# Performance work log

Hardware: AMD Instinct MI355X
Metric: run time of the kernel (lower is better)

## Reference

```python
import jax, jax.numpy as jnp
import numpy as np

KERNEL_SIZES = [1, 2, 3]
KERNEL_NUM = 11
SIGMA = 0.1
EXACT_SIGMA = 0.001
EMBED_DIM = 300
HIDDEN = 128
Q_VOCAB = 30000
D_VOCAB = 30000


def _mus_sigmas():
    mus, sigmas = [], []
    K = KERNEL_NUM
    for i in range(K):
        mu = 1.0 / (K - 1) + 2.0 * i / (K - 1) - 1.0
        sigma = SIGMA
        if mu > 1.0:
            sigma = EXACT_SIGMA
            mu = 1.0
        mus.append(mu)
        sigmas.append(sigma)
    return jnp.asarray(mus, jnp.float32), jnp.asarray(sigmas, jnp.float32)


def _conv_tanh(x_bcl, w, b, ks):
    # x_bcl: (B, C_in, L); ConstantPad1d((0, ks)) + Conv1d(kernel=ks+1) keeps length L
    y = jax.lax.conv_general_dilated(
        x_bcl, w, window_strides=(1,), padding=[(0, ks)],
        dimension_numbers=('NCW', 'OIW', 'NCW'))
    return jnp.tanh(y + b[None, :, None])  # (B, H, L)


def _l2norm(x):
    n = jnp.sqrt(jnp.sum(x * x, axis=-1, keepdims=True))
    return x / jnp.maximum(n, 1e-12)


def setup_inputs() -> dict:
    key = jax.random.key(0)
    ks = jax.random.split(key, 16)
    inp = {
        'query': jax.random.randint(ks[0], (128, 128), 0, Q_VOCAB),
        'doc': jax.random.randint(ks[1], (128, 512), 0, D_VOCAB),
        'q_emb': jax.random.normal(ks[2], (Q_VOCAB, EMBED_DIM), jnp.float32) * 0.1,
        'd_emb': jax.random.normal(ks[3], (D_VOCAB, EMBED_DIM), jnp.float32) * 0.1,
        'out_w': jax.random.normal(ks[4], (1, 3 * 3 * KERNEL_NUM), jnp.float32) * 0.1,
        'out_b': jnp.zeros((1,), jnp.float32),
    }
    for idx, k in enumerate(KERNEL_SIZES):
        fan_in = EMBED_DIM * (k + 1)
        inp[f'conv_w{idx}'] = jax.random.normal(ks[5 + 2 * idx], (HIDDEN, EMBED_DIM, k + 1), jnp.float32) / np.sqrt(fan_in)
        inp[f'conv_b{idx}'] = jnp.zeros((HIDDEN,), jnp.float32)
    return inp


def reference(query, doc, q_emb, d_emb, conv_w0, conv_b0, conv_w1, conv_b1,
              conv_w2, conv_b2, out_w, out_b):
    mus, sigmas = _mus_sigmas()
    inv2s2 = 1.0 / (2.0 * sigmas * sigmas)  # (K,)

    q_e = q_emb[query].transpose(0, 2, 1)  # (B, D, Lq)
    d_e = d_emb[doc].transpose(0, 2, 1)    # (B, D, Ld)

    cws = [(conv_w0, conv_b0), (conv_w1, conv_b1), (conv_w2, conv_b2)]
    # q_convs/d_convs share weights (same nn.Sequential appended to both lists)
    q_convs = [_l2norm(_conv_tanh(q_e, w, b, ks).transpose(0, 2, 1))
               for (w, b), ks in zip(cws, KERNEL_SIZES)]  # each (B, Lq, H)
    d_convs = [_l2norm(_conv_tanh(d_e, w, b, ks).transpose(0, 2, 1))
               for (w, b), ks in zip(cws, KERNEL_SIZES)]  # each (B, Ld, H)

    KM = []
    for qi in range(3):
        for di in range(3):
            mm = jnp.einsum('bld,brd->blr', q_convs[qi], d_convs[di])  # (B,Lq,Ld)
            # Gaussian kernel soft-histogram, vectorized over all kernels
            kern = jnp.exp(-(mm[..., None] - mus) ** 2 * inv2s2)  # (B,Lq,Ld,K)
            K = jnp.log1p(kern.sum(axis=2)).sum(axis=1)           # (B,K)
            KM.append(K)
    phi = jnp.concatenate(KM, axis=1)  # (B, 9*KERNEL_NUM)
    return phi @ out_w.T + out_b       # (B, 1)
```

## Files before the change

kernel.cpp:

```cpp
#include <hip/hip_runtime.h>
#include <hip/hip_bf16.h>

typedef __hip_bfloat16 bf16;
typedef __attribute__((ext_vector_type(8))) short short8;
typedef __attribute__((ext_vector_type(4))) float f32x4;
typedef __attribute__((ext_vector_type(2))) float f32x2;

#define NB 128
#define NH 128
#define NLQ 128
#define NLD 512
#define NEMB 300
#define XQROWS 132
#define XDROWS 516
#define XCOLS 320

__device__ __forceinline__ unsigned short bfbits(float x) {
    __hip_bfloat16 h = __float2bfloat16(x);
    return *reinterpret_cast<unsigned short*>(&h);
}

__device__ __forceinline__ float fast_tanh(float x) {
    x = fminf(9.f, fmaxf(-9.f, x));
    float e = __builtin_amdgcn_exp2f(x * 2.8853900817779268f);
    return (e - 1.f) * __builtin_amdgcn_rcpf(e + 1.f);
}

__global__ __launch_bounds__(256)
void pack_all(const int* __restrict__ q_tok, const int* __restrict__ d_tok,
              const float* __restrict__ q_emb, const float* __restrict__ d_emb,
              const float* __restrict__ cw0, const float* __restrict__ cw1,
              const float* __restrict__ cw2,
              bf16* __restrict__ Wp, bf16* __restrict__ Xq, bf16* __restrict__ Xd)
{
    int bx = blockIdx.x;
    if (bx < 1440) {
        int e = bx * 256 + threadIdx.x;
        int widx = (e >= 204800) ? 2 : (e >= 81920 ? 1 : 0);
        int off = (widx == 0) ? 0 : (widx == 1 ? 81920 : 204800);
        int el = e - off;
        int W = widx + 2;
        int ch = el >> 12;
        int cc = ch / W;
        int t  = ch - cc * W;
        int h  = (el >> 5) & 127;
        int cp = el & 31;
        int c  = cc * 32 + cp;
        const float* cw = (widx == 0) ? cw0 : (widx == 1 ? cw1 : cw2);
        float v = (c < NEMB) ? cw[(h * NEMB + c) * W + t] : 0.f;
        Wp[e] = __float2bfloat16(v);
        return;
    }
    int gid = (bx - 1440) * 256 + threadIdx.x;
    int row = gid / 20, g = gid - row * 20;
    const float* emb; bf16* dst; int tok;
    if (row < NB * XQROWS) {
        int b = row / XQROWS, l = row - b * XQROWS;
        tok = (l < NLQ) ? q_tok[b * NLQ + l] : -1;
        emb = q_emb;
        dst = Xq + (size_t)row * XCOLS + g * 16;
    } else {
        int rowd = row - NB * XQROWS;
        int b = rowd / XDROWS, l = rowd - b * XDROWS;
        tok = (l < NLD) ? d_tok[b * NLD + l] : -1;
        emb = d_emb;
        dst = Xd + (size_t)rowd * XCOLS + g * 16;
    }
    int c0 = g * 16;
    float4 v[4];
    #pragma unroll
    for (int q = 0; q < 4; ++q) {
        int c = c0 + q * 4;
        v[q] = make_float4(0.f, 0.f, 0.f, 0.f);
        if (tok >= 0 && c < NEMB)
            v[q] = *reinterpret_cast<const float4*>(emb + (size_t)tok * NEMB + c);
    }
    short8 o0, o1;
    o0[0] = (short)bfbits(v[0].x); o0[1] = (short)bfbits(v[0].y);
    o0[2] = (short)bfbits(v[0].z); o0[3] = (short)bfbits(v[0].w);
    o0[4] = (short)bfbits(v[1].x); o0[5] = (short)bfbits(v[1].y);
    o0[6] = (short)bfbits(v[1].z); o0[7] = (short)bfbits(v[1].w);
    o1[0] = (short)bfbits(v[2].x); o1[1] = (short)bfbits(v[2].y);
    o1[2] = (short)bfbits(v[2].z); o1[3] = (short)bfbits(v[2].w);
    o1[4] = (short)bfbits(v[3].x); o1[5] = (short)bfbits(v[3].y);
    o1[6] = (short)bfbits(v[3].z); o1[7] = (short)bfbits(v[3].w);
    *reinterpret_cast<short8*>(dst) = o0;
    *reinterpret_cast<short8*>(dst + 8) = o1;
}

__global__ __launch_bounds__(512, 4)
void conv_kernel(const bf16* __restrict__ Xq, const bf16* __restrict__ Xd,
                 const bf16* __restrict__ Wp,
                 const float* __restrict__ cb0, const float* __restrict__ cb1,
                 const float* __restrict__ cb2,
                 bf16* __restrict__ qn, bf16* __restrict__ dn)
{
    __shared__ bf16 Xs[2][2][132][40];
    __shared__ bf16 Bs[2][128][36];
    __shared__ float ssq[2][256];

    int bx = blockIdx.x;
    int widx = bx % 3;
    int inner = bx / 3;
    int W = widx + 2;
    const bf16* wp = Wp + ((widx == 0) ? 0 : (widx == 1 ? 81920 : 204800));
    const float* cb = (widx == 0) ? cb0 : (widx == 1 ? cb1 : cb2);

    int tid = threadIdx.x;
    int lane = tid & 63;
    int wv = tid >> 6;
    int wr = wv >> 1;
    int wc = wv & 1;
    int s_wave = wr >> 1;
    int lr_base = (wr & 1) * 64;

    bf16* outp; int L;
    int sb0, sb1, sl00, sl01;
    const bf16* xbase;
    size_t grow0, grow1;
    if (inner < 64) {
        outp = qn + (size_t)widx * NB * NLQ * NH;
        L = NLQ; sb0 = inner * 2; sb1 = sb0 + 1; sl00 = 0; sl01 = 0;
        xbase = Xq; grow0 = (size_t)sb0 * XQROWS; grow1 = (size_t)sb1 * XQROWS;
    } else {
        int i = inner - 64;
        outp = dn + (size_t)widx * NB * NLD * NH;
        L = NLD; sb0 = i >> 1; sb1 = sb0; sl00 = (i & 1) * 256; sl01 = sl00 + 128;
        xbase = Xd; grow0 = (size_t)sb0 * XDROWS + sl00; grow1 = grow0 + 128;
    }

    int sr = tid >> 2;
    int colg = tid & 3;
    const bf16* gsrc0 = xbase + (grow0 + sr) * XCOLS + colg * 8;
    const bf16* gsrc1 = xbase + (grow1 + sr) * XCOLS + colg * 8;
    bool has_tail = (tid >= 448 && tid < 480);
    int j = tid - 448;
    int ts = (j >> 2) >> 2, trr = 128 + ((j >> 2) & 3), tcolg = j & 3;
    const bf16* gsrcT = xbase + ((ts ? grow1 : grow0) + trr) * XCOLS + tcolg * 8;

    const short8* wp8 = reinterpret_cast<const short8*>(wp);
    int bh = tid >> 2, bcg = tid & 3;

    {
        short8 a0 = *reinterpret_cast<const short8*>(gsrc0);
        short8 a1 = *reinterpret_cast<const short8*>(gsrc1);
        short8 at;
        if (has_tail) at = *reinterpret_cast<const short8*>(gsrcT);
        short8 b0 = wp8[tid];
        *reinterpret_cast<short8*>(&Xs[0][0][sr][colg * 8]) = a0;
        *reinterpret_cast<short8*>(&Xs[0][1][sr][colg * 8]) = a1;
        if (has_tail) *reinterpret_cast<short8*>(&Xs[0][ts][trr][tcolg * 8]) = at;
        *reinterpret_cast<short8*>(&Bs[0][bh][bcg * 8]) = b0;
    }
    __syncthreads();

    f32x4 acc[4][4];
    #pragma unroll
    for (int m = 0; m < 4; ++m)
        #pragma unroll
        for (int n = 0; n < 4; ++n)
            acc[m][n] = (f32x4){0.f, 0.f, 0.f, 0.f};

    int nsteps = W * 10;
    int xcur = 0, bcur = 0, step = 0;
    short8 a0, a1, at;
    for (int cc = 0; cc < 10; ++cc) {
        if (cc < 9) {
            a0 = *reinterpret_cast<const short8*>(gsrc0 + (cc + 1) * 32);
            a1 = *reinterpret_cast<const short8*>(gsrc1 + (cc + 1) * 32);
            if (has_tail) at = *reinterpret_cast<const short8*>(gsrcT + (cc + 1) * 32);
        }
        for (int t = 0; t < W; ++t, ++step) {
            short8 nb;
            bool hn = (step + 1 < nsteps);
            if (hn) nb = wp8[(size_t)(step + 1) * 512 + tid];

            short8 bv[4], af[4];
            #pragma unroll
            for (int n = 0; n < 4; ++n)
                bv[n] = *reinterpret_cast<const short8*>(
                    &Bs[bcur][wc * 64 + n * 16 + (lane & 15)][(lane >> 4) * 8]);
            #pragma unroll
            for (int m = 0; m < 4; ++m)
                af[m] = *reinterpret_cast<const short8*>(
                    &Xs[xcur][s_wave][lr_base + m * 16 + (lane & 15) + t][(lane >> 4) * 8]);
            #pragma unroll
            for (int m = 0; m < 4; ++m)
                #pragma unroll
                for (int n = 0; n < 4; ++n)
                    acc[m][n] = __builtin_amdgcn_mfma_f32_16x16x32_bf16(af[m], bv[n], acc[m][n], 0, 0, 0);

            if (hn)
                *reinterpret_cast<short8*>(&Bs[bcur ^ 1][bh][bcg * 8]) = nb;
            if (t == W - 1 && cc < 9) {
                *reinterpret_cast<short8*>(&Xs[xcur ^ 1][0][sr][colg * 8]) = a0;
                *reinterpret_cast<short8*>(&Xs[xcur ^ 1][1][sr][colg * 8]) = a1;
                if (has_tail) *reinterpret_cast<short8*>(&Xs[xcur ^ 1][ts][trr][tcolg * 8]) = at;
            }
            if (hn || (t == W - 1 && cc < 9)) __syncthreads();
            bcur ^= 1;
            if (t == W - 1) xcur ^= 1;
        }
    }

    float ssl[4][4];
    #pragma unroll
    for (int m = 0; m < 4; ++m)
        #pragma unroll
        for (int i = 0; i < 4; ++i) ssl[m][i] = 0.f;

    #pragma unroll
    for (int n = 0; n < 4; ++n) {
        float bias = cb[wc * 64 + n * 16 + (lane & 15)];
        #pragma unroll
        for (int m = 0; m < 4; ++m)
            #pragma unroll
            for (int i = 0; i < 4; ++i) {
                float v = fast_tanh(acc[m][n][i] + bias);
                acc[m][n][i] = v;
                ssl[m][i] += v * v;
            }
    }
    #pragma unroll
    for (int m = 0; m < 4; ++m)
        #pragma unroll
        for (int i = 0; i < 4; ++i) {
            float s = ssl[m][i];
            s += __shfl_xor(s, 1); s += __shfl_xor(s, 2);
            s += __shfl_xor(s, 4); s += __shfl_xor(s, 8);
            ssl[m][i] = s;
        }
    if ((lane & 15) == 0) {
        #pragma unroll
        for (int m = 0; m < 4; ++m)
            #pragma unroll
            for (int i = 0; i < 4; ++i)
                ssq[wc][wr * 64 + m * 16 + (lane >> 4) * 4 + i] = ssl[m][i];
    }
    __syncthreads();
    #pragma unroll
    for (int m = 0; m < 4; ++m)
        #pragma unroll
        for (int i = 0; i < 4; ++i) {
            int r = wr * 64 + m * 16 + (lane >> 4) * 4 + i;
            float s2 = ssq[0][r] + ssq[1][r];
            float sc = 1.f / fmaxf(sqrtf(s2), 1e-12f);
            int s = r >> 7, lr = r & 127;
            int b = s ? sb1 : sb0;
            int l = (s ? sl01 : sl00) + lr;
            bf16* dst = outp + ((size_t)(b * L + l)) * NH;
            #pragma unroll
            for (int n = 0; n < 4; ++n)
                dst[wc * 64 + n * 16 + (lane & 15)] = __float2bfloat16(acc[m][n][i] * sc);
        }
}

__global__ __launch_bounds__(512, 4)
void sim_kernel(const bf16* __restrict__ qn, const bf16* __restrict__ dn,
                float* __restrict__ phi_part)
{
    __shared__ bf16 QDs[2][64][136];
    bf16* flat = &QDs[0][0][0];
    float (*red)[64][11] = reinterpret_cast<float(*)[64][11]>(flat);

    int blk = blockIdx.x;
    int b = blk / 18;
    int rem = blk - b * 18;
    int pair = rem >> 1;
    int half = rem & 1;
    int qi = pair / 3, di = pair - qi * 3;

    int tid = threadIdx.x, lane = tid & 63, wv = tid >> 6;
    int wr = wv >> 2;
    int wc = wv & 3;

    const bf16* qbase = qn + ((size_t)qi * NB + b) * (NLQ * NH) + (size_t)half * 64 * NH;
    const bf16* dbase = dn + ((size_t)di * NB + b) * (NLD * NH);

    {
        int r = tid >> 3, h0 = (tid & 7) * 16;
        *reinterpret_cast<short8*>(flat + r * 136 + h0) =
            *reinterpret_cast<const short8*>(qbase + (size_t)r * NH + h0);
        *reinterpret_cast<short8*>(flat + r * 136 + h0 + 8) =
            *reinterpret_cast<const short8*>(qbase + (size_t)r * NH + h0 + 8);
    }
    __syncthreads();

    short8 bq[4];
    #pragma unroll
    for (int kc = 0; kc < 4; ++kc)
        bq[kc] = *reinterpret_cast<const short8*>(
            flat + (wc * 16 + (lane & 15)) * 136 + kc * 32 + (lane >> 4) * 8);
    __syncthreads();

    int dr = tid >> 3, dc = (tid & 7) * 16;
    {
        short8 st0 = *reinterpret_cast<const short8*>(dbase + (size_t)dr * NH + dc);
        short8 st1 = *reinterpret_cast<const short8*>(dbase + (size_t)dr * NH + dc + 8);
        *reinterpret_cast<short8*>(&QDs[0][dr][dc]) = st0;
        *reinterpret_cast<short8*>(&QDs[0][dr][dc + 8]) = st1;
    }
    __syncthreads();

    f32x2 sums2[11];
    #pragma unroll
    for (int k = 0; k < 11; ++k) sums2[k] = (f32x2){0.f, 0.f};

    int cur = 0;
    for (int cc = 0; cc < 8; ++cc) {
        short8 st0, st1;
        if (cc < 7) {
            st0 = *reinterpret_cast<const short8*>(dbase + (size_t)((cc + 1) * 64 + dr) * NH + dc);
            st1 = *reinterpret_cast<const short8*>(dbase + (size_t)((cc + 1) * 64 + dr) * NH + dc + 8);
        }

        f32x4 acc[2];
        acc[0] = (f32x4){0.f, 0.f, 0.f, 0.f};
        acc[1] = (f32x4){0.f, 0.f, 0.f, 0.f};

        #pragma unroll
        for (int kc = 0; kc < 4; ++kc) {
            short8 af[2];
            #pragma unroll
            for (int m = 0; m < 2; ++m)
                af[m] = *reinterpret_cast<const short8*>(
                    &QDs[cur][wr * 32 + m * 16 + (lane & 15)][kc * 32 + (lane >> 4) * 8]);
            #pragma unroll
            for (int m = 0; m < 2; ++m)
                acc[m] = __builtin_amdgcn_mfma_f32_16x16x32_bf16(af[m], bq[kc], acc[m], 0, 0, 0);
        }

        if (cc < 7) {
            *reinterpret_cast<short8*>(&QDs[cur ^ 1][dr][dc]) = st0;
            *reinterpret_cast<short8*>(&QDs[cur ^ 1][dr][dc + 8]) = st1;
        }

        f32x2 cmax = (f32x2){-2.f, -2.f};
        #pragma unroll
        for (int i = 0; i < 4; ++i) {
            f32x2 x2;
            x2.x = acc[0][i];
            x2.y = acc[1][i];
            cmax.x = fmaxf(cmax.x, x2.x);
            cmax.y = fmaxf(cmax.y, x2.y);
            f32x2 ax = x2 * 28.853900817779268f;
            f32x2 R, Ri, E4;
            R.x = __builtin_amdgcn_exp2f(ax.x);
            R.y = __builtin_amdgcn_exp2f(ax.y);
            Ri.x = __builtin_amdgcn_exp2f(-ax.x);
            Ri.y = __builtin_amdgcn_exp2f(-ax.y);
            f32x2 d4 = x2 + 0.1f;
            f32x2 t = d4 * d4 * (-72.134752044448169f);
            E4.x = __builtin_amdgcn_exp2f(t.x);
            E4.y = __builtin_amdgcn_exp2f(t.y);
            sums2[4] += E4;
            f32x2 u = E4 * R;
            sums2[5] += u;
            u *= R; sums2[6] += u;
            u *= R; sums2[7] += u;
            u *= R; sums2[8] += u;
            u *= R; sums2[9] += u;
            f32x2 w = E4 * Ri;
            sums2[3] += w;
            w *= Ri; sums2[2] += w;
            w *= Ri; sums2[1] += w;
            w *= Ri; sums2[0] += w;
        }
        if (__any(fmaxf(cmax.x, cmax.y) > 0.98f)) {
            #pragma unroll
            for (int i = 0; i < 4; ++i) {
                f32x2 x2;
                x2.x = acc[0][i];
                x2.y = acc[1][i];
                f32x2 d1 = x2 - 1.0f;
                f32x2 t1 = d1 * d1 * (-721347.52044448f);
                f32x2 e;
                e.x = __builtin_amdgcn_exp2f(t1.x);
                e.y = __builtin_amdgcn_exp2f(t1.y);
                sums2[10] += e;
            }
        }

        __syncthreads();
        cur ^= 1;
    }

    #pragma unroll
    for (int k = 0; k < 11; ++k) {
        float s = sums2[k].x + sums2[k].y;
        s += __shfl_xor(s, 16);
        s += __shfl_xor(s, 32);
        sums2[k].x = s;
    }
    if ((lane >> 4) == 0) {
        #pragma unroll
        for (int k = 0; k < 11; ++k)
            red[wr][wc * 16 + (lane & 15)][k] = sums2[k].x;
    }
    __syncthreads();

    if (tid < 64) {
        const float scale[11] = {
            4.2483542552915889e-18f,
            3.7751345442790977e-11f,
            6.1442123533282098e-6f,
            1.8315638888734179e-2f,
            1.f, 1.f,
            1.8315638888734179e-2f,
            6.1442123533282098e-6f,
            3.7751345442790977e-11f,
            4.2483542552915889e-18f,
            1.f };
        float lv[11];
        #pragma unroll
        for (int k = 0; k < 11; ++k)
            lv[k] = log1pf(scale[k] * (red[0][tid][k] + red[1][tid][k]));
        #pragma unroll
        for (int k = 0; k < 11; ++k) {
            float s = lv[k];
            s += __shfl_xor(s, 1); s += __shfl_xor(s, 2); s += __shfl_xor(s, 4);
            s += __shfl_xor(s, 8); s += __shfl_xor(s, 16); s += __shfl_xor(s, 32);
            lv[k] = s;
        }
        if (tid == 0) {
            #pragma unroll
            for (int k = 0; k < 11; ++k)
                phi_part[(size_t)blk * 11 + k] = lv[k];
        }
    }
}

__global__ void final_kernel(const float* __restrict__ phi_part,
                             const float* __restrict__ ow,
                             const float* __restrict__ obias, float* __restrict__ out)
{
    int b = threadIdx.x;
    float s = obias[0];
    #pragma unroll
    for (int pair = 0; pair < 9; ++pair)
        #pragma unroll
        for (int k = 0; k < 11; ++k) {
            size_t base = ((size_t)b * 18 + pair * 2) * 11 + k;
            s += (phi_part[base] + phi_part[base + 11]) * ow[pair * 11 + k];
        }
    out[b] = s;
}

extern "C" void kernel_launch(void* const* d_in, const int* in_sizes, int n_in,
                              void* d_out, int out_size, void* d_ws, size_t ws_size,
                              hipStream_t stream)
{
    const int*   query = (const int*)d_in[0];
    const int*   doc   = (const int*)d_in[1];
    const float* q_emb = (const float*)d_in[2];
    const float* d_emb = (const float*)d_in[3];
    const float* out_w = (const float*)d_in[4];
    const float* out_b = (const float*)d_in[5];
    const float* cw0 = (const float*)d_in[6];
    const float* cb0 = (const float*)d_in[7];
    const float* cw1 = (const float*)d_in[8];
    const float* cb1 = (const float*)d_in[9];
    const float* cw2 = (const float*)d_in[10];
    const float* cb2 = (const float*)d_in[11];

    const size_t QN = (size_t)NB * NLQ * NH;
    const size_t DN = (size_t)NB * NLD * NH;
    const size_t XQN = (size_t)NB * XQROWS * XCOLS;
    const size_t XDN = (size_t)NB * XDROWS * XCOLS;

    bf16* Wp = (bf16*)d_ws;
    bf16* Xq = Wp + 368640;
    bf16* Xd = Xq + XQN;
    bf16* qn = Xd + XDN;
    bf16* dn = qn + 3 * QN;
    float* phi_part = (float*)(dn + 3 * DN);

    pack_all<<<7920, 256, 0, stream>>>(query, doc, q_emb, d_emb, cw0, cw1, cw2, Wp, Xq, Xd);
    conv_kernel<<<960, 512, 0, stream>>>(Xq, Xd, Wp, cb0, cb1, cb2, qn, dn);
    sim_kernel<<<NB * 9 * 2, 512, 0, stream>>>(qn, dn, phi_part);
    final_kernel<<<1, 128, 0, stream>>>(phi_part, out_w, out_b, (float*)d_out);
}
```

Before: 204.5 us.

## Software-pipeline kernel pooling against next chunk's MFMA with dual accumulators

Restructures the doc-chunk loop so that the MFMA for chunk i+1 is issued before the Gaussian-kernel pooling of chunk i. Two accumulator sets (accA/accB) alternate, and the loop is manually unrolled by two. The aim is to overlap the exp-heavy VALU pooling with matrix-core work. The global-to-LDS staging load is now issued and stored back to back rather than spanning the MFMA. This may expose global latency, and it raises register pressure from the extra accumulators.

```diff
diff --git a/kernel.cpp b/kernel.cpp
--- a/kernel.cpp
+++ b/kernel.cpp
@@ -306,41 +306,26 @@
     #pragma unroll
     for (int k = 0; k < 11; ++k) sums2[k] = (f32x2){0.f, 0.f};
 
-    int cur = 0;
-    for (int cc = 0; cc < 8; ++cc) {
-        short8 st0, st1;
-        if (cc < 7) {
-            st0 = *reinterpret_cast<const short8*>(dbase + (size_t)((cc + 1) * 64 + dr) * NH + dc);
-            st1 = *reinterpret_cast<const short8*>(dbase + (size_t)((cc + 1) * 64 + dr) * NH + dc + 8);
-        }
-
-        f32x4 acc[2];
-        acc[0] = (f32x4){0.f, 0.f, 0.f, 0.f};
-        acc[1] = (f32x4){0.f, 0.f, 0.f, 0.f};
-
+    auto do_mfma = [&](int cur, f32x4* acc2) {
+        acc2[0] = (f32x4){0.f, 0.f, 0.f, 0.f};
+        acc2[1] = (f32x4){0.f, 0.f, 0.f, 0.f};
         #pragma unroll
         for (int kc = 0; kc < 4; ++kc) {
-            short8 af[2];
-            #pragma unroll
-            for (int m = 0; m < 2; ++m)
-                af[m] = *reinterpret_cast<const short8*>(
-                    &QDs[cur][wr * 32 + m * 16 + (lane & 15)][kc * 32 + (lane >> 4) * 8]);
-            #pragma unroll
-            for (int m = 0; m < 2; ++m)
-                acc[m] = __builtin_amdgcn_mfma_f32_16x16x32_bf16(af[m], bq[kc], acc[m], 0, 0, 0);
-        }
-
-        if (cc < 7) {
-            *reinterpret_cast<short8*>(&QDs[cur ^ 1][dr][dc]) = st0;
-            *reinterpret_cast<short8*>(&QDs[cur ^ 1][dr][dc + 8]) = st1;
-        }
-
+            short8 af0 = *reinterpret_cast<const short8*>(
+                &QDs[cur][wr * 32 + (lane & 15)][kc * 32 + (lane >> 4) * 8]);
+            short8 af1 = *reinterpret_cast<const short8*>(
+                &QDs[cur][wr * 32 + 16 + (lane & 15)][kc * 32 + (lane >> 4) * 8]);
+            acc2[0] = __builtin_amdgcn_mfma_f32_16x16x32_bf16(af0, bq[kc], acc2[0], 0, 0, 0);
+            acc2[1] = __builtin_amdgcn_mfma_f32_16x16x32_bf16(af1, bq[kc], acc2[1], 0, 0, 0);
+        }
+    };
+    auto do_pool = [&](const f32x4* acc2) {
         f32x2 cmax = (f32x2){-2.f, -2.f};
         #pragma unroll
         for (int i = 0; i < 4; ++i) {
             f32x2 x2;
-            x2.x = acc[0][i];
-            x2.y = acc[1][i];
+            x2.x = acc2[0][i];
+            x2.y = acc2[1][i];
             cmax.x = fmaxf(cmax.x, x2.x);
             cmax.y = fmaxf(cmax.y, x2.y);
             f32x2 ax = x2 * 28.853900817779268f;
@@ -370,8 +355,8 @@
             #pragma unroll
             for (int i = 0; i < 4; ++i) {
                 f32x2 x2;
-                x2.x = acc[0][i];
-                x2.y = acc[1][i];
+                x2.x = acc2[0][i];
+                x2.y = acc2[1][i];
                 f32x2 d1 = x2 - 1.0f;
                 f32x2 t1 = d1 * d1 * (-721347.52044448f);
                 f32x2 e;
@@ -380,10 +365,37 @@
                 sums2[10] += e;
             }
         }
-
+    };
+    auto stage_next = [&](int cc, int cur) {
+        short8 st0 = *reinterpret_cast<const short8*>(dbase + (size_t)((cc + 1) * 64 + dr) * NH + dc);
+        short8 st1 = *reinterpret_cast<const short8*>(dbase + (size_t)((cc + 1) * 64 + dr) * NH + dc + 8);
+        *reinterpret_cast<short8*>(&QDs[cur ^ 1][dr][dc]) = st0;
+        *reinterpret_cast<short8*>(&QDs[cur ^ 1][dr][dc + 8]) = st1;
+    };
+
+    f32x4 accA[2], accB[2];
+
+    do_mfma(0, accA);
+    stage_next(0, 0);
+    __syncthreads();
+    int cur = 1;
+
+    #pragma unroll
+    for (int it = 1; it < 8; it += 2) {
+        do_mfma(cur, accB);
+        if (it < 7) stage_next(it, cur);
+        do_pool(accA);
         __syncthreads();
         cur ^= 1;
-    }
+        if (it + 1 < 8) {
+            do_mfma(cur, accA);
+            if (it + 1 < 7) stage_next(it + 1, cur);
+            do_pool(accB);
+            __syncthreads();
+            cur ^= 1;
+        }
+    }
+    do_pool(accB);
 
     #pragma unroll
     for (int k = 0; k < 11; ++k) {
```

Measured after the change: 340.0 us. 1.66x slower.
